# Performance work log

Measured on AMD Instinct MI355X. Metric: run time of the kernel, lower is better.

The kernel has to match this reference:

```python
import jax, jax.numpy as jnp
import numpy as np

GAMMA = 2.0
ASPECT_W = 1.0
OPINION_W = 1.0
SENTIMENT_W = 1.0
BOUNDARY_W = 0.5
IGNORE = -100

B, S, C_SPAN, C_SENT = 256, 8192, 3, 3


def setup_inputs() -> dict:
    key = jax.random.key(0)
    k1, k2, k3, k4, k5, k6, k7 = jax.random.split(key, 7)
    return {
        "aspect_logits": jax.random.normal(k1, (B, S, C_SPAN), dtype=jnp.float32),
        "opinion_logits": jax.random.normal(k2, (B, S, C_SPAN), dtype=jnp.float32),
        "sentiment_logits": jax.random.normal(k3, (B, C_SENT), dtype=jnp.float32),
        "boundary_logits": jax.random.normal(k4, (B, S, 2), dtype=jnp.float32),
        "aspect_labels": jax.random.randint(k5, (B, S), 0, 3, dtype=jnp.int32),
        "opinion_labels": jax.random.randint(k6, (B, S), 0, 3, dtype=jnp.int32),
        "sentiment_labels": jax.random.randint(k7, (B,), 0, 3, dtype=jnp.int32),
    }


def _masked_ce(logits2d, labels1d):
    """Per-position CE with ignore_index=-100; returns (ce, valid_mask)."""
    valid = labels1d != IGNORE
    safe = jnp.where(valid, labels1d, 0)
    logp = jax.nn.log_softmax(logits2d, axis=-1)
    ce = -jnp.take_along_axis(logp, safe[:, None], axis=-1)[:, 0]
    ce = jnp.where(valid, ce, 0.0)
    return ce, valid


def _focal_loss(logits, labels, gamma):
    C = logits.shape[-1]
    ce, valid = _masked_ce(logits.reshape(-1, C), labels.reshape(-1))
    pt = jnp.exp(-ce)
    fl = (1.0 - pt) ** gamma * ce
    n = valid.sum().astype(fl.dtype)
    return jnp.where(n > 0, fl.sum() / jnp.maximum(n, 1.0), 0.0)


def _boundary_labels(span_labels):
    """Vectorized version of the per-batch Python-loop boundary construction.
    start: label==1; end: label==2 and next label != 2 (last pos counts if ==2)."""
    start = (span_labels == 1)
    nxt = jnp.concatenate(
        [span_labels[:, 1:], jnp.full_like(span_labels[:, :1], -1)], axis=1)
    end = (span_labels == 2) & (nxt != 2)
    return start, end


def reference(aspect_logits, opinion_logits, sentiment_logits, boundary_logits,
              aspect_labels, opinion_labels, sentiment_labels):
    # focal span losses
    aspect_loss = _focal_loss(aspect_logits, aspect_labels, GAMMA)
    opinion_loss = _focal_loss(opinion_logits, opinion_labels, GAMMA)

    # sentiment CE (mean over valid)
    ce_s, valid_s = _masked_ce(sentiment_logits, sentiment_labels)
    n_s = valid_s.sum().astype(ce_s.dtype)
    sentiment_loss = ce_s.sum() / jnp.maximum(n_s, 1.0)

    # boundary labels: OR of aspect/opinion starts and ends
    a_start, a_end = _boundary_labels(aspect_labels)
    o_start, o_end = _boundary_labels(opinion_labels)
    start = (a_start | o_start).astype(boundary_logits.dtype)
    end = (a_end | o_end).astype(boundary_logits.dtype)
    y = jnp.stack([start, end], axis=-1)  # [B, S, 2]

    z = boundary_logits
    bce = jnp.maximum(z, 0.0) - z * y + jnp.log1p(jnp.exp(-jnp.abs(z)))
    boundary_loss = bce.mean()

    total = (ASPECT_W * aspect_loss + OPINION_W * opinion_loss +
             SENTIMENT_W * sentiment_loss + BOUNDARY_W * boundary_loss)
    return total
```

## Files before the change

kernel.cpp:

```cpp
#include <hip/hip_runtime.h>

constexpr int BB = 256;
constexpr int SS = 8192;
constexpr int NPOS = BB * SS;
constexpr int IGNORE = -100;
constexpr int BLOCKS = NPOS / 4 / 256;

__device__ __forceinline__ void focal_acc(float l0, float l1, float l2,
                                          int lab, float& fl, float& cnt) {
    if (lab == IGNORE) return;
    float m   = fmaxf(l0, fmaxf(l1, l2));
    float s   = __expf(l0 - m) + __expf(l1 - m) + __expf(l2 - m);
    float lse = m + __logf(s);
    float x   = (lab == 0) ? l0 : ((lab == 1) ? l1 : l2);
    float ce  = lse - x;
    float pt  = __expf(-ce);
    float om  = 1.0f - pt;
    fl  += om * om * ce;
    cnt += 1.0f;
}

__device__ __forceinline__ float bce_term(float z, float y) {
    return fmaxf(z, 0.0f) - z * y + __logf(1.0f + __expf(-fabsf(z)));
}

__global__ __launch_bounds__(256)
void main_kernel(const float* __restrict__ a_logits,
                 const float* __restrict__ o_logits,
                 const float* __restrict__ b_logits,
                 const int*   __restrict__ a_labels,
                 const int*   __restrict__ o_labels,
                 float*       __restrict__ partial) {
    int t = blockIdx.x * blockDim.x + threadIdx.x;
    float fl_a = 0.f, cnt_a = 0.f, fl_o = 0.f, cnt_o = 0.f, bce = 0.f;

    {
        int p0 = t * 4;
        int lane = threadIdx.x & 63;

        int4 al4 = *(const int4*)(a_labels + p0);
        int4 ol4 = *(const int4*)(o_labels + p0);

        int al_next = __shfl_down(al4.x, 1, 64);
        int ol_next = __shfl_down(ol4.x, 1, 64);
        if (lane == 63) {
            if (((p0 + 3) & (SS - 1)) != SS - 1) {
                al_next = a_labels[p0 + 4];
                ol_next = o_labels[p0 + 4];
            } else {
                al_next = -1;
                ol_next = -1;
            }
        }
        int al[5] = {al4.x, al4.y, al4.z, al4.w, al_next};
        int ol[5] = {ol4.x, ol4.y, ol4.z, ol4.w, ol_next};

        const float4* ap = (const float4*)(a_logits + p0 * 3);
        const float4* op = (const float4*)(o_logits + p0 * 3);
        float4 A0 = ap[0], A1 = ap[1], A2 = ap[2];
        float4 O0 = op[0], O1 = op[1], O2 = op[2];
        float aL[12] = {A0.x, A0.y, A0.z, A0.w, A1.x, A1.y, A1.z, A1.w,
                        A2.x, A2.y, A2.z, A2.w};
        float oL[12] = {O0.x, O0.y, O0.z, O0.w, O1.x, O1.y, O1.z, O1.w,
                        O2.x, O2.y, O2.z, O2.w};

        const float4* bp = (const float4*)(b_logits + p0 * 2);
        float4 Z0 = bp[0], Z1 = bp[1];
        float z[8] = {Z0.x, Z0.y, Z0.z, Z0.w, Z1.x, Z1.y, Z1.z, Z1.w};

        #pragma unroll
        for (int j = 0; j < 4; ++j) {
            focal_acc(aL[3*j], aL[3*j+1], aL[3*j+2], al[j], fl_a, cnt_a);
            focal_acc(oL[3*j], oL[3*j+1], oL[3*j+2], ol[j], fl_o, cnt_o);
            float ys = ((al[j] == 1) || (ol[j] == 1)) ? 1.0f : 0.0f;
            float ye = (((al[j] == 2) && (al[j+1] != 2)) ||
                        ((ol[j] == 2) && (ol[j+1] != 2))) ? 1.0f : 0.0f;
            bce += bce_term(z[2*j],     ys);
            bce += bce_term(z[2*j + 1], ye);
        }
    }

    float vals[5] = {fl_a, cnt_a, fl_o, cnt_o, bce};
    #pragma unroll
    for (int k = 0; k < 5; ++k) {
        float v = vals[k];
        #pragma unroll
        for (int o = 32; o > 0; o >>= 1) v += __shfl_down(v, o, 64);
        vals[k] = v;
    }
    __shared__ float lds[4 * 5];
    int lane = threadIdx.x & 63, wid = threadIdx.x >> 6;
    if (lane == 0) {
        #pragma unroll
        for (int k = 0; k < 5; ++k) lds[wid * 5 + k] = vals[k];
    }
    __syncthreads();
    if (threadIdx.x == 0) {
        #pragma unroll
        for (int k = 0; k < 5; ++k) {
            float s = lds[k] + lds[5 + k] + lds[10 + k] + lds[15 + k];
            partial[k * BLOCKS + blockIdx.x] = s;
        }
    }
}

__global__ __launch_bounds__(256)
void sent_final_kernel(const float* __restrict__ s_logits,
                       const int*   __restrict__ s_labels,
                       const float* __restrict__ partial,
                       float* __restrict__ out) {
    int tid = threadIdx.x;

    float acc[5];
    #pragma unroll
    for (int k = 0; k < 5; ++k) {
        float s = 0.f;
        #pragma unroll
        for (int i = 0; i < BLOCKS / 256; ++i)
            s += partial[k * BLOCKS + tid + i * 256];
        acc[k] = s;
    }

    float ce = 0.f, cnt = 0.f;
    {
        int lab = s_labels[tid];
        if (lab != IGNORE) {
            float l0 = s_logits[3*tid], l1 = s_logits[3*tid+1], l2 = s_logits[3*tid+2];
            float m   = fmaxf(l0, fmaxf(l1, l2));
            float lse = m + __logf(__expf(l0-m) + __expf(l1-m) + __expf(l2-m));
            float x   = (lab == 0) ? l0 : ((lab == 1) ? l1 : l2);
            ce  = lse - x;
            cnt = 1.0f;
        }
    }

    float vals[7] = {acc[0], acc[1], acc[2], acc[3], acc[4], ce, cnt};
    #pragma unroll
    for (int k = 0; k < 7; ++k) {
        float v = vals[k];
        #pragma unroll
        for (int o = 32; o > 0; o >>= 1) v += __shfl_down(v, o, 64);
        vals[k] = v;
    }
    __shared__ float lds[4 * 7];
    int lane = threadIdx.x & 63, wid = threadIdx.x >> 6;
    if (lane == 0) {
        #pragma unroll
        for (int k = 0; k < 7; ++k) lds[wid * 7 + k] = vals[k];
    }
    __syncthreads();
    if (threadIdx.x == 0) {
        float tot[7];
        #pragma unroll
        for (int k = 0; k < 7; ++k)
            tot[k] = lds[k] + lds[7 + k] + lds[14 + k] + lds[21 + k];
        double fl_a = tot[0], ca = tot[1], fl_o = tot[2], co = tot[3];
        double bsum = tot[4], sv = tot[5], sc = tot[6];
        double aspect  = (ca > 0.0) ? fl_a / fmax(ca, 1.0) : 0.0;
        double opinion = (co > 0.0) ? fl_o / fmax(co, 1.0) : 0.0;
        double senti   = sv / fmax(sc, 1.0);
        double bnd     = bsum / (double)((long long)NPOS * 2);
        out[0] = (float)(aspect + opinion + senti + 0.5 * bnd);
    }
}

extern "C" void kernel_launch(void* const* d_in, const int* in_sizes, int n_in,
                              void* d_out, int out_size, void* d_ws, size_t ws_size,
                              hipStream_t stream) {
    const float* a_logits = (const float*)d_in[0];
    const float* o_logits = (const float*)d_in[1];
    const float* s_logits = (const float*)d_in[2];
    const float* b_logits = (const float*)d_in[3];
    const int*   a_labels = (const int*)d_in[4];
    const int*   o_labels = (const int*)d_in[5];
    const int*   s_labels = (const int*)d_in[6];
    float* out = (float*)d_out;
    float* partial = (float*)d_ws;

    main_kernel<<<BLOCKS, 256, 0, stream>>>(a_logits, o_logits, b_logits,
                                            a_labels, o_labels, partial);
    sent_final_kernel<<<1, 256, 0, stream>>>(s_logits, s_labels, partial, out);
}
```

Before: 115.4 us.

## Use nontemporal vector loads, cheaper focal pt, and wider final reduction

All streaming loads of logits and labels now use nontemporal builtin loads, and they are issued before the neighbour-label shuffle. The focal term computes pt as the label's softmax numerator times a hardware reciprocal of the sum, replacing a second exp. The final reduction kernel runs with 1024 threads so each thread sums fewer partials. The cost being targeted is cache pollution and instruction latency in a bandwidth-bound kernel, plus the serial tail of the single-block final reduction. The reciprocal approximation slightly changes numerics.

New measurement: 127.6 us. +10.6%, slower.

```diff
diff --git a/kernel.cpp b/kernel.cpp
--- a/kernel.cpp
+++ b/kernel.cpp
@@ -6,16 +6,25 @@
 constexpr int IGNORE = -100;
 constexpr int BLOCKS = NPOS / 4 / 256;
 
+typedef float f32x4 __attribute__((ext_vector_type(4)));
+typedef int   i32x4 __attribute__((ext_vector_type(4)));
+
+template <typename T>
+__device__ __forceinline__ T ntload(const T* p) {
+    return __builtin_nontemporal_load(p);
+}
+
 __device__ __forceinline__ void focal_acc(float l0, float l1, float l2,
                                           int lab, float& fl, float& cnt) {
     if (lab == IGNORE) return;
-    float m   = fmaxf(l0, fmaxf(l1, l2));
-    float s   = __expf(l0 - m) + __expf(l1 - m) + __expf(l2 - m);
-    float lse = m + __logf(s);
-    float x   = (lab == 0) ? l0 : ((lab == 1) ? l1 : l2);
-    float ce  = lse - x;
-    float pt  = __expf(-ce);
-    float om  = 1.0f - pt;
+    float m  = fmaxf(l0, fmaxf(l1, l2));
+    float e0 = __expf(l0 - m), e1 = __expf(l1 - m), e2 = __expf(l2 - m);
+    float s  = e0 + e1 + e2;
+    float x  = (lab == 0) ? l0 : ((lab == 1) ? l1 : l2);
+    float el = (lab == 0) ? e0 : ((lab == 1) ? e1 : e2);
+    float ce = __logf(s) + (m - x);
+    float pt = el * __builtin_amdgcn_rcpf(s);
+    float om = 1.0f - pt;
     fl  += om * om * ce;
     cnt += 1.0f;
 }
@@ -35,14 +44,20 @@
     float fl_a = 0.f, cnt_a = 0.f, fl_o = 0.f, cnt_o = 0.f, bce = 0.f;
 
     {
-        int p0 = t * 4;
+        int p0   = t * 4;
         int lane = threadIdx.x & 63;
 
-        int4 al4 = *(const int4*)(a_labels + p0);
-        int4 ol4 = *(const int4*)(o_labels + p0);
+        i32x4 al4 = ntload((const i32x4*)(a_labels + p0));
+        i32x4 ol4 = ntload((const i32x4*)(o_labels + p0));
+        const f32x4* ap = (const f32x4*)(a_logits + p0 * 3);
+        const f32x4* op = (const f32x4*)(o_logits + p0 * 3);
+        const f32x4* bp = (const f32x4*)(b_logits + p0 * 2);
+        f32x4 A0 = ntload(ap),     A1 = ntload(ap + 1), A2 = ntload(ap + 2);
+        f32x4 O0 = ntload(op),     O1 = ntload(op + 1), O2 = ntload(op + 2);
+        f32x4 Z0 = ntload(bp),     Z1 = ntload(bp + 1);
 
-        int al_next = __shfl_down(al4.x, 1, 64);
-        int ol_next = __shfl_down(ol4.x, 1, 64);
+        int al_next = __shfl_down(al4[0], 1, 64);
+        int ol_next = __shfl_down(ol4[0], 1, 64);
         if (lane == 63) {
             if (((p0 + 3) & (SS - 1)) != SS - 1) {
                 al_next = a_labels[p0 + 4];
@@ -52,21 +67,14 @@
                 ol_next = -1;
             }
         }
-        int al[5] = {al4.x, al4.y, al4.z, al4.w, al_next};
-        int ol[5] = {ol4.x, ol4.y, ol4.z, ol4.w, ol_next};
+        int al[5] = {al4[0], al4[1], al4[2], al4[3], al_next};
+        int ol[5] = {ol4[0], ol4[1], ol4[2], ol4[3], ol_next};
 
-        const float4* ap = (const float4*)(a_logits + p0 * 3);
-        const float4* op = (const float4*)(o_logits + p0 * 3);
-        float4 A0 = ap[0], A1 = ap[1], A2 = ap[2];
-        float4 O0 = op[0], O1 = op[1], O2 = op[2];
-        float aL[12] = {A0.x, A0.y, A0.z, A0.w, A1.x, A1.y, A1.z, A1.w,
-                        A2.x, A2.y, A2.z, A2.w};
-        float oL[12] = {O0.x, O0.y, O0.z, O0.w, O1.x, O1.y, O1.z, O1.w,
-                        O2.x, O2.y, O2.z, O2.w};
-
-        const float4* bp = (const float4*)(b_logits + p0 * 2);
-        float4 Z0 = bp[0], Z1 = bp[1];
-        float z[8] = {Z0.x, Z0.y, Z0.z, Z0.w, Z1.x, Z1.y, Z1.z, Z1.w};
+        float aL[12] = {A0[0], A0[1], A0[2], A0[3], A1[0], A1[1], A1[2], A1[3],
+                        A2[0], A2[1], A2[2], A2[3]};
+        float oL[12] = {O0[0], O0[1], O0[2], O0[3], O1[0], O1[1], O1[2], O1[3],
+                        O2[0], O2[1], O2[2], O2[3]};
+        float z[8]   = {Z0[0], Z0[1], Z0[2], Z0[3], Z1[0], Z1[1], Z1[2], Z1[3]};
 
         #pragma unroll
         for (int j = 0; j < 4; ++j) {
@@ -104,7 +112,7 @@
     }
 }
 
-__global__ __launch_bounds__(256)
+__global__ __launch_bounds__(1024)
 void sent_final_kernel(const float* __restrict__ s_logits,
                        const int*   __restrict__ s_labels,
                        const float* __restrict__ partial,
@@ -116,13 +124,13 @@
     for (int k = 0; k < 5; ++k) {
         float s = 0.f;
         #pragma unroll
-        for (int i = 0; i < BLOCKS / 256; ++i)
-            s += partial[k * BLOCKS + tid + i * 256];
+        for (int i = 0; i < BLOCKS / 1024; ++i)
+            s += partial[k * BLOCKS + tid + i * 1024];
         acc[k] = s;
     }
 
     float ce = 0.f, cnt = 0.f;
-    {
+    if (tid < BB) {
         int lab = s_labels[tid];
         if (lab != IGNORE) {
             float l0 = s_logits[3*tid], l1 = s_logits[3*tid+1], l2 = s_logits[3*tid+2];
@@ -142,7 +150,7 @@
         for (int o = 32; o > 0; o >>= 1) v += __shfl_down(v, o, 64);
         vals[k] = v;
     }
-    __shared__ float lds[4 * 7];
+    __shared__ float lds[16 * 7];
     int lane = threadIdx.x & 63, wid = threadIdx.x >> 6;
     if (lane == 0) {
         #pragma unroll
@@ -152,8 +160,12 @@
     if (threadIdx.x == 0) {
         float tot[7];
         #pragma unroll
-        for (int k = 0; k < 7; ++k)
-            tot[k] = lds[k] + lds[7 + k] + lds[14 + k] + lds[21 + k];
+        for (int k = 0; k < 7; ++k) {
+            float s = 0.f;
+            #pragma unroll
+            for (int w = 0; w < 16; ++w) s += lds[w * 7 + k];
+            tot[k] = s;
+        }
         double fl_a = tot[0], ca = tot[1], fl_o = tot[2], co = tot[3];
         double bsum = tot[4], sv = tot[5], sc = tot[6];
         double aspect  = (ca > 0.0) ? fl_a / fmax(ca, 1.0) : 0.0;
@@ -179,5 +191,5 @@
 
     main_kernel<<<BLOCKS, 256, 0, stream>>>(a_logits, o_logits, b_logits,
                                             a_labels, o_labels, partial);
-    sent_final_kernel<<<1, 256, 0, stream>>>(s_logits, s_labels, partial, out);
+    sent_final_kernel<<<1, 1024, 0, stream>>>(s_logits, s_labels, partial, out);
 }
```
